# Kernel tuning notes

Measured on AMD Instinct MI355X. Metric: run time of the kernel, lower is better.

## Reference

```python
import jax, jax.numpy as jnp
import numpy as np

N_SPLIT = 4096   # split tokens (coarse octree levels)
N_VQ    = 12288  # VQ tokens (finest level)
N       = N_SPLIT + N_VQ
C       = 256    # num_embed
H       = 8      # num_heads
L       = 4      # num_blocks
P       = 256    # patch_size (attention window)
DIL     = 2      # dilation for odd (swin) blocks
DVQ     = 32     # vqvae embedding_channels
VQ_SIZE = 256    # vqvae embedding_sizes
VQ_G    = 4      # vqvae quantizer_group
HID     = 4 * C


def _layernorm(x, s, b):
    m = x.mean(-1, keepdims=True)
    v = jnp.var(x, axis=-1, keepdims=True)
    return (x - m) * jax.lax.rsqrt(v + 1e-5) * s + b


def _sin_pos_emb(n, c):
    pos = jnp.arange(n, dtype=jnp.float32)[:, None]
    half = c // 2
    freqs = jnp.exp(-jnp.log(10000.0) * jnp.arange(half, dtype=jnp.float32) / half)
    ang = pos * freqs
    return jnp.concatenate([jnp.sin(ang), jnp.cos(ang)], axis=-1)


def _forward(split, zq, targets_vq, category, batch_id, mask, d2b,
             split_emb, class_emb, vq_proj_w, vq_proj_b,
             ln1_s, ln1_b, qkv_w, qkv_b, attn_w, attn_b,
             ln2_s, ln2_b, fc1_w, fc1_b, fc2_w, fc2_b,
             lnx_s, lnx_b, split_w, split_b, vq_w, vq_b):
    # token embeddings: [split tokens ; projected VQ codes]
    x = jnp.concatenate([split_emb[split], zq @ vq_proj_w + vq_proj_b], axis=0)  # [N,C]
    cond = class_emb[category]                      # [B,C]
    x = jnp.where(mask[:, None], cond[batch_id], x)  # masked tokens -> class cond

    # depth2batch gather, then OctFormer blocks
    xb = x[d2b] + _sin_pos_emb(N, C).astype(x.dtype)
    dh = C // H
    scale = dh ** -0.5
    for l in range(L):
        d = DIL if (l % 2 == 1) else 1  # swin-style alternating dilation
        h = _layernorm(xb, ln1_s[l], ln1_b[l])
        # dilated window partition: window j in a super-window holds tokens base+p*d+j
        hw = h.reshape(-1, P, d, C).transpose(0, 2, 1, 3).reshape(-1, P, C)
        qkv = hw @ qkv_w[l] + qkv_b[l]              # [nw,P,3C]
        q, k, v = [t.reshape(-1, P, H, dh) for t in jnp.split(qkv, 3, axis=-1)]
        att = jax.nn.softmax(jnp.einsum('wphd,wqhd->whpq', q, k) * scale, axis=-1)
        o = jnp.einsum('whpq,wqhd->wphd', att, v).reshape(-1, P, C) @ attn_w[l] + attn_b[l]
        o = o.reshape(-1, d, P, C).transpose(0, 2, 1, 3).reshape(-1, C)  # undo partition
        xb = xb + o
        h = _layernorm(xb, ln2_s[l], ln2_b[l])
        xb = xb + (jax.nn.gelu(h @ fc1_w[l] + fc1_b[l]) @ fc2_w[l] + fc2_b[l])
    # batch2depth scatter (inverse permutation)
    x = jnp.zeros_like(xb).at[d2b].set(xb)
    x = _layernorm(x, lnx_s, lnx_b)

    # split head + masked cross-entropy
    sl = x[:N_SPLIT] @ split_w + split_b            # [Ns,2]
    ms = mask[:N_SPLIT].astype(jnp.float32)
    ce_s = -jnp.take_along_axis(jax.nn.log_softmax(sl, axis=-1), split[:, None], axis=-1)[:, 0]
    split_loss = jnp.sum(ce_s * ms) / jnp.maximum(jnp.sum(ms), 1.0)

    # vq head + masked grouped cross-entropy
    vl = (x[N_SPLIT:] @ vq_w + vq_b).reshape(N_VQ, VQ_G, VQ_SIZE)
    mv = mask[N_SPLIT:].astype(jnp.float32)
    ce_v = -jnp.take_along_axis(jax.nn.log_softmax(vl, axis=-1), targets_vq[..., None], axis=-1)[..., 0]
    vq_loss = jnp.sum(ce_v.mean(-1) * mv) / jnp.maximum(jnp.sum(mv), 1.0)
    return jnp.stack([split_loss, vq_loss])


def setup_inputs() -> dict:
    key = jax.random.key(0)
    ks = jax.random.split(key, 16)
    s = 0.02
    inp = {
        'split': jax.random.randint(ks[0], (N_SPLIT,), 0, 2),
        'zq': jax.random.normal(ks[1], (N_VQ, DVQ), jnp.float32),
        'targets_vq': jax.random.randint(ks[2], (N_VQ, VQ_G), 0, VQ_SIZE),
        'category': jnp.zeros((1,), jnp.int32),
        'batch_id': jnp.zeros((N,), jnp.int32),
        'mask': jax.random.randint(ks[3], (N,), 0, 2).astype(bool),
        'd2b': jax.random.permutation(ks[4], N),
        'split_emb': s * jax.random.normal(ks[5], (2, C), jnp.float32),
        'class_emb': s * jax.random.normal(ks[6], (1, C), jnp.float32),
        'vq_proj_w': s * jax.random.normal(ks[7], (DVQ, C), jnp.float32),
        'vq_proj_b': jnp.zeros((C,), jnp.float32),
        'ln1_s': jnp.ones((L, C), jnp.float32),
        'ln1_b': jnp.zeros((L, C), jnp.float32),
        'qkv_w': s * jax.random.normal(ks[8], (L, C, 3 * C), jnp.float32),
        'qkv_b': jnp.zeros((L, 3 * C), jnp.float32),
        'attn_w': s * jax.random.normal(ks[9], (L, C, C), jnp.float32),
        'attn_b': jnp.zeros((L, C), jnp.float32),
        'ln2_s': jnp.ones((L, C), jnp.float32),
        'ln2_b': jnp.zeros((L, C), jnp.float32),
        'fc1_w': s * jax.random.normal(ks[10], (L, C, HID), jnp.float32),
        'fc1_b': jnp.zeros((L, HID), jnp.float32),
        'fc2_w': s * jax.random.normal(ks[11], (L, HID, C), jnp.float32),
        'fc2_b': jnp.zeros((L, C), jnp.float32),
        'lnx_s': jnp.ones((C,), jnp.float32),
        'lnx_b': jnp.zeros((C,), jnp.float32),
        'split_w': s * jax.random.normal(ks[12], (C, 2), jnp.float32),
        'split_b': jnp.zeros((2,), jnp.float32),
        'vq_w': s * jax.random.normal(ks[13], (C, VQ_G * VQ_SIZE), jnp.float32),
        'vq_b': jnp.zeros((VQ_G * VQ_SIZE,), jnp.float32),
    }
    return inp


def reference(split, zq, targets_vq, category, batch_id, mask, d2b,
              split_emb, class_emb, vq_proj_w, vq_proj_b,
              ln1_s, ln1_b, qkv_w, qkv_b, attn_w, attn_b,
              ln2_s, ln2_b, fc1_w, fc1_b, fc2_w, fc2_b,
              lnx_s, lnx_b, split_w, split_b, vq_w, vq_b):
    return _forward(split, zq, targets_vq, category, batch_id, mask, d2b,
                    split_emb, class_emb, vq_proj_w, vq_proj_b,
                    ln1_s, ln1_b, qkv_w, qkv_b, attn_w, attn_b,
                    ln2_s, ln2_b, fc1_w, fc1_b, fc2_w, fc2_b,
                    lnx_s, lnx_b, split_w, split_b, vq_w, vq_b)
```

## Files before the change

### kernel.cpp

```cpp
#include <hip/hip_runtime.h>
#include <hip/hip_bf16.h>
#include <math.h>

#define NSPLIT 4096
#define NVQ    12288
#define NTOK   16384
#define CH     256
#define NH     8
#define DHD    32
#define NL     4
#define PW     256
#define HIDN   1024
#define DVQ    32
#define VQG    4
#define VQS    256

typedef __attribute__((ext_vector_type(8))) short bf16x8;
typedef __attribute__((ext_vector_type(4))) float f32x4;

typedef const __attribute__((address_space(1))) void* gas_ptr;
typedef __attribute__((address_space(3))) void* las_ptr;
#define GLD16(g, s) __builtin_amdgcn_global_load_lds((gas_ptr)(g), (las_ptr)(s), 16, 0, 0)

static __device__ __forceinline__ unsigned pack2bf(float a, float b) {
    __hip_bfloat16 ha = __float2bfloat16(a), hb = __float2bfloat16(b);
    return ((unsigned)*(unsigned short*)&hb << 16) | *(unsigned short*)&ha;
}
static __device__ __forceinline__ float bf2f(unsigned short s) {
    unsigned u = (unsigned)s << 16;
    return *(float*)&u;
}
static __device__ __forceinline__ unsigned short f2bfu(float f) {
    __hip_bfloat16 h = __float2bfloat16(f);
    return *(unsigned short*)&h;
}

__global__ void k_wt_all(const float* __restrict__ qkv_w, const float* __restrict__ attn_w,
                         const float* __restrict__ fc1_w, const float* __restrict__ fc2_w,
                         const float* __restrict__ vq_w,
                         short* __restrict__ qkvT, short* __restrict__ attnT,
                         short* __restrict__ fc1T, short* __restrict__ fc2T,
                         short* __restrict__ vqT,
                         const void* __restrict__ mask_raw, int* __restrict__ mode) {
    int b = blockIdx.x;
    if (b == 832) {
        __shared__ int c_even, c_odd, c_0100;
        const unsigned short* u16 = (const unsigned short*)mask_raw;
        if (threadIdx.x == 0) { c_even = 0; c_odd = 0; c_0100 = 0; }
        __syncthreads();
        int le = 0, lo = 0, l01 = 0;
        for (int i = threadIdx.x; i < 8192; i += 256) {
            unsigned short v = u16[i];
            if (v == 0x3F80u) { if (i & 1) lo++; else le++; }
            if (v == 0x0100u) l01++;
        }
        atomicAdd(&c_even, le); atomicAdd(&c_odd, lo); atomicAdd(&c_0100, l01);
        __syncthreads();
        if (threadIdx.x == 0) {
            int m;
            if      (c_even > 500) m = 2;
            else if (c_odd  > 500) m = 3;
            else if (c_0100 > 500) m = 1;
            else                   m = 0;
            *mode = m;
        }
        return;
    }
    const float* W; short* Wt; int K, N, tn, tk;
    if (b < 192)      { int r = b;       int z = r / 48; r %= 48; K = 256;  N = 768;
                        tk = r / 12; tn = r % 12;
                        W = qkv_w + (size_t)z * K * N; Wt = qkvT + (size_t)z * K * N; }
    else if (b < 256) { int r = b - 192; int z = r / 16; r %= 16; K = 256;  N = 256;
                        tk = r / 4;  tn = r % 4;
                        W = attn_w + (size_t)z * K * N; Wt = attnT + (size_t)z * K * N; }
    else if (b < 512) { int r = b - 256; int z = r / 64; r %= 64; K = 256;  N = 1024;
                        tk = r / 16; tn = r % 16;
                        W = fc1_w + (size_t)z * K * N; Wt = fc1T + (size_t)z * K * N; }
    else if (b < 768) { int r = b - 512; int z = r / 64; r %= 64; K = 1024; N = 256;
                        tk = r / 4;  tn = r % 4;
                        W = fc2_w + (size_t)z * K * N; Wt = fc2T + (size_t)z * K * N; }
    else              { int r = b - 768; K = 256; N = 1024;
                        tk = r / 16; tn = r % 16; W = vq_w; Wt = vqT; }
    __shared__ float t[64][65];
    int bn = tn * 64, bk = tk * 64, tid = threadIdx.x;
#pragma unroll
    for (int it = 0; it < 16; ++it) {
        int idx = it * 256 + tid; int r = idx >> 6, c = idx & 63;
        t[r][c] = W[(size_t)(bk + r) * N + bn + c];
    }
    __syncthreads();
#pragma unroll
    for (int it = 0; it < 16; ++it) {
        int idx = it * 256 + tid; int r = idx >> 6, c = idx & 63;
        __hip_bfloat16 h = __float2bfloat16(t[c][r]);
        Wt[(size_t)(bn + r) * K + bk + c] = *(short*)&h;
    }
}

__global__ void k_embed_gather(const int* __restrict__ split, const float* __restrict__ zq,
                               const int* __restrict__ category, const int* __restrict__ batch_id,
                               const void* __restrict__ mask_raw, const int* __restrict__ mode,
                               int* __restrict__ mask_i, const int* __restrict__ d2b,
                               const float* __restrict__ split_emb, const float* __restrict__ class_emb,
                               const float* __restrict__ vq_proj_w, const float* __restrict__ vq_proj_b,
                               const float* __restrict__ ln1s, const float* __restrict__ ln1b,
                               unsigned short* __restrict__ xbv, unsigned short* __restrict__ hb) {
    int j = blockIdx.x, c = threadIdx.x;
    int i = d2b[j];
    int m = *mode, mv;
    if      (m == 0) mv = ((const int*)mask_raw)[i] != 0;
    else if (m == 1) mv = ((const unsigned char*)mask_raw)[i] != 0;
    else if (m == 2) mv = ((const unsigned short*)mask_raw)[i] != 0;
    else             mv = ((const unsigned int*)mask_raw)[i] != 0;
    if (c == 0) mask_i[i] = mv;
    float v;
    if (mv) {
        v = class_emb[category[batch_id[i]] * CH + c];
    } else if (i < NSPLIT) {
        v = split_emb[split[i] * CH + c];
    } else {
        const float* z = zq + (size_t)(i - NSPLIT) * DVQ;
        float acc = vq_proj_b[c];
#pragma unroll
        for (int k = 0; k < DVQ; k++) acc += z[k] * vq_proj_w[k * CH + c];
        v = acc;
    }
    const float kneg = -0.07195578415606394f;
    float jf = (float)j, pe;
    if (c < 128) { float f = expf(c * kneg);         pe = sinf(jf * f); }
    else         { float f = expf((c - 128) * kneg); pe = cosf(jf * f); }
    v += pe;
    float s = v, sq = v * v;
#pragma unroll
    for (int o = 32; o; o >>= 1) { s += __shfl_xor(s, o); sq += __shfl_xor(sq, o); }
    __shared__ float ps[4], pq[4];
    if ((c & 63) == 0) { ps[c >> 6] = s; pq[c >> 6] = sq; }
    __syncthreads();
    float S = ps[0] + ps[1] + ps[2] + ps[3];
    float Q = pq[0] + pq[1] + pq[2] + pq[3];
    float mean = S * (1.0f / CH);
    float var  = Q * (1.0f / CH) - mean * mean;
    float rsf = rsqrtf(var + 1e-5f);
    xbv[(size_t)j * CH + c] = f2bfu(v);
    hb[(size_t)j * CH + c]  = f2bfu((v - mean) * rsf * ln1s[c] + ln1b[c]);
}

template <int GELU>
__global__ __launch_bounds__(256, 4) void k_mm(
    const short* __restrict__ A, const short* __restrict__ Bt,
    const float* __restrict__ bias, unsigned short* __restrict__ outB,
    int N, int K) {
    __shared__ short As[2][128 * 32];
    __shared__ short Bs[2][128 * 32];
    const int tid = threadIdx.x;
    const int w = tid >> 6, l = tid & 63;
    const int bm = blockIdx.y * 128, bn = blockIdx.x * 128;
    const int wr = w >> 1, wc = w & 1;
    const int q = l >> 4, rA = l & 15;
    const int srow = w * 16 + (l >> 2);
    const int sx = ((l & 3) ^ ((l >> 2) & 3)) * 8;
    const int fx = (q ^ (rA & 3)) * 8;

    const short* gA0 = A + (size_t)(bm + srow) * K + sx;
    const short* gA1 = A + (size_t)(bm + srow + 64) * K + sx;
    const short* gB0 = Bt + (size_t)(bn + srow) * K + sx;
    const short* gB1 = Bt + (size_t)(bn + srow + 64) * K + sx;
    short* lA0 = &As[0][w * 16 * 32];
    short* lA1 = &As[0][(64 + w * 16) * 32];
    short* lA0h = &As[1][w * 16 * 32];
    short* lA1h = &As[1][(64 + w * 16) * 32];
    short* lB0 = &Bs[0][w * 16 * 32];
    short* lB1 = &Bs[0][(64 + w * 16) * 32];
    short* lB0h = &Bs[1][w * 16 * 32];
    short* lB1h = &Bs[1][(64 + w * 16) * 32];

    f32x4 acc[4][4] = {};

    for (int k0 = 0; k0 < K; k0 += 64) {
        GLD16(gA0 + k0, lA0);       GLD16(gA1 + k0, lA1);
        GLD16(gA0 + k0 + 32, lA0h); GLD16(gA1 + k0 + 32, lA1h);
        GLD16(gB0 + k0, lB0);       GLD16(gB1 + k0, lB1);
        GLD16(gB0 + k0 + 32, lB0h); GLD16(gB1 + k0 + 32, lB1h);
        __syncthreads();
#pragma unroll
        for (int s = 0; s < 2; s++) {
            bf16x8 a[4], b[4];
#pragma unroll
            for (int m = 0; m < 4; m++)
                a[m] = *(const bf16x8*)(&As[s][(wr * 64 + m * 16 + rA) * 32 + fx]);
#pragma unroll
            for (int n = 0; n < 4; n++)
                b[n] = *(const bf16x8*)(&Bs[s][(wc * 64 + n * 16 + rA) * 32 + fx]);
#pragma unroll
            for (int m = 0; m < 4; m++)
#pragma unroll
                for (int n = 0; n < 4; n++)
                    acc[m][n] = __builtin_amdgcn_mfma_f32_16x16x32_bf16(b[n], a[m], acc[m][n], 0, 0, 0);
        }
        __syncthreads();
    }

#pragma unroll
    for (int m = 0; m < 4; m++) {
        int row = bm + wr * 64 + m * 16 + rA;
#pragma unroll
        for (int n = 0; n < 4; n++) {
            int colb = bn + wc * 64 + n * 16 + q * 4;
            float4 bv = *(const float4*)(bias + colb);
            float v0 = acc[m][n][0] + bv.x;
            float v1 = acc[m][n][1] + bv.y;
            float v2 = acc[m][n][2] + bv.z;
            float v3 = acc[m][n][3] + bv.w;
            if (GELU) {
                float t0 = tanhf(0.7978845608028654f * (v0 + 0.044715f * v0 * v0 * v0));
                float t1 = tanhf(0.7978845608028654f * (v1 + 0.044715f * v1 * v1 * v1));
                float t2 = tanhf(0.7978845608028654f * (v2 + 0.044715f * v2 * v2 * v2));
                float t3 = tanhf(0.7978845608028654f * (v3 + 0.044715f * v3 * v3 * v3));
                v0 = 0.5f * v0 * (1.0f + t0); v1 = 0.5f * v1 * (1.0f + t1);
                v2 = 0.5f * v2 * (1.0f + t2); v3 = 0.5f * v3 * (1.0f + t3);
            }
            ushort4 st = { f2bfu(v0), f2bfu(v1), f2bfu(v2), f2bfu(v3) };
            *(ushort4*)(outB + (size_t)row * N + colb) = st;
        }
    }
}

template <int LNOUT>
__global__ __launch_bounds__(256, 4) void k_mm_row(
    const short* __restrict__ A, const short* __restrict__ Bt,
    const float* __restrict__ bias, unsigned short* __restrict__ xbv,
    const float* __restrict__ lns, const float* __restrict__ lnb,
    unsigned short* __restrict__ h_out, const int* __restrict__ d2b, int K) {
    __shared__ short As[2][32 * 32];
    __shared__ short Bs[2][256 * 32];
    __shared__ float part[2][4][32];
    const int tid = threadIdx.x;
    const int w = tid >> 6, l = tid & 63;
    const int bm = blockIdx.x * 32;
    const int q = l >> 4, rA = l & 15;
    const int sx = ((l & 3) ^ ((l >> 2) & 3)) * 8;
    const int fx = (q ^ (rA & 3)) * 8;

    const short* gA = A + (size_t)(bm + (l >> 2)) * K + sx;
    const short* gB = Bt + (size_t)(w * 64 + (l >> 2)) * K + sx;

    f32x4 acc[2][4] = {};

    for (int k0 = 0; k0 < K; k0 += 64) {
        if (w == 0) {
#pragma unroll
            for (int rg = 0; rg < 2; rg++) {
                GLD16(gA + (size_t)(rg * 16) * K + k0,      &As[0][(rg * 16) * 32]);
                GLD16(gA + (size_t)(rg * 16) * K + k0 + 32, &As[1][(rg * 16) * 32]);
            }
        }
#pragma unroll
        for (int i = 0; i < 4; i++) {
            GLD16(gB + (size_t)(i * 16) * K + k0,      &Bs[0][(w * 64 + i * 16) * 32]);
            GLD16(gB + (size_t)(i * 16) * K + k0 + 32, &Bs[1][(w * 64 + i * 16) * 32]);
        }
        __syncthreads();
#pragma unroll
        for (int s = 0; s < 2; s++) {
            bf16x8 a[2], b[4];
#pragma unroll
            for (int m = 0; m < 2; m++)
                a[m] = *(const bf16x8*)(&As[s][(m * 16 + rA) * 32 + fx]);
#pragma unroll
            for (int n = 0; n < 4; n++)
                b[n] = *(const bf16x8*)(&Bs[s][(w * 64 + n * 16 + rA) * 32 + fx]);
#pragma unroll
            for (int m = 0; m < 2; m++)
#pragma unroll
                for (int n = 0; n < 4; n++)
                    acc[m][n] = __builtin_amdgcn_mfma_f32_16x16x32_bf16(b[n], a[m], acc[m][n], 0, 0, 0);
        }
        __syncthreads();
    }

    float rsum[2] = {}, rsq[2] = {};
#pragma unroll
    for (int m = 0; m < 2; m++) {
        int row = bm + m * 16 + rA;
#pragma unroll
        for (int n = 0; n < 4; n++) {
            int colb = w * 64 + n * 16 + q * 4;
            float4 bv = *(const float4*)(bias + colb);
            size_t oi = (size_t)row * CH + colb;
            ushort4 xo = *(const ushort4*)(xbv + oi);
            float v0 = acc[m][n][0] + bv.x + bf2f(xo.x);
            float v1 = acc[m][n][1] + bv.y + bf2f(xo.y);
            float v2 = acc[m][n][2] + bv.z + bf2f(xo.z);
            float v3 = acc[m][n][3] + bv.w + bf2f(xo.w);
            acc[m][n][0] = v0; acc[m][n][1] = v1; acc[m][n][2] = v2; acc[m][n][3] = v3;
            if (LNOUT != 2) {
                ushort4 st = { f2bfu(v0), f2bfu(v1), f2bfu(v2), f2bfu(v3) };
                *(ushort4*)(xbv + oi) = st;
            }
            rsum[m] += (v0 + v1) + (v2 + v3);
            rsq[m]  += (v0 * v0 + v1 * v1) + (v2 * v2 + v3 * v3);
        }
    }
    if (LNOUT) {
#pragma unroll
        for (int m = 0; m < 2; m++) {
            rsum[m] += __shfl_xor(rsum[m], 16); rsum[m] += __shfl_xor(rsum[m], 32);
            rsq[m]  += __shfl_xor(rsq[m], 16);  rsq[m]  += __shfl_xor(rsq[m], 32);
        }
        if (q == 0) {
#pragma unroll
            for (int m = 0; m < 2; m++) {
                part[0][w][m * 16 + rA] = rsum[m];
                part[1][w][m * 16 + rA] = rsq[m];
            }
        }
        __syncthreads();
#pragma unroll
        for (int m = 0; m < 2; m++) {
            int row = m * 16 + rA;
            float S = part[0][0][row] + part[0][1][row] + part[0][2][row] + part[0][3][row];
            float Q = part[1][0][row] + part[1][1][row] + part[1][2][row] + part[1][3][row];
            float mean = S * (1.0f / CH);
            float var  = Q * (1.0f / CH) - mean * mean;
            float rsf = rsqrtf(var + 1e-5f);
            size_t orow = (LNOUT == 2) ? (size_t)d2b[bm + row] : (size_t)(bm + row);
#pragma unroll
            for (int n = 0; n < 4; n++) {
                int colb = w * 64 + n * 16 + q * 4;
                float4 sv = *(const float4*)(lns + colb);
                float4 bb = *(const float4*)(lnb + colb);
                ushort4 st = {
                    f2bfu((acc[m][n][0] - mean) * rsf * sv.x + bb.x),
                    f2bfu((acc[m][n][1] - mean) * rsf * sv.y + bb.y),
                    f2bfu((acc[m][n][2] - mean) * rsf * sv.z + bb.z),
                    f2bfu((acc[m][n][3] - mean) * rsf * sv.w + bb.w) };
                *(ushort4*)(h_out + orow * CH + colb) = st;
            }
        }
    }
}

__global__ __launch_bounds__(256, 4) void k_vq_head(
    const short* __restrict__ A, const short* __restrict__ vqT,
    const float* __restrict__ vq_b, const int* __restrict__ targets,
    float* __restrict__ vce4) {
    __shared__ short As[2][32 * 32];
    __shared__ short Bs[2][256 * 32];
    __shared__ float part[2][4][32];
    __shared__ float tgtv[32];
    const int tid = threadIdx.x;
    const int w = tid >> 6, l = tid & 63;
    const int bm = blockIdx.x * 32;
    const int g = blockIdx.y;
    const int q = l >> 4, rA = l & 15;
    const int sx = ((l & 3) ^ ((l >> 2) & 3)) * 8;
    const int fx = (q ^ (rA & 3)) * 8;

    const short* gA = A + (size_t)(bm + (l >> 2)) * CH + sx;
    const short* gB = vqT + (size_t)(g * VQS + w * 64 + (l >> 2)) * CH + sx;

    f32x4 acc[2][4] = {};

    for (int k0 = 0; k0 < CH; k0 += 64) {
        if (w == 0) {
#pragma unroll
            for (int rg = 0; rg < 2; rg++) {
                GLD16(gA + (size_t)(rg * 16) * CH + k0,      &As[0][(rg * 16) * 32]);
                GLD16(gA + (size_t)(rg * 16) * CH + k0 + 32, &As[1][(rg * 16) * 32]);
            }
        }
#pragma unroll
        for (int i = 0; i < 4; i++) {
            GLD16(gB + (size_t)(i * 16) * CH + k0,      &Bs[0][(w * 64 + i * 16) * 32]);
            GLD16(gB + (size_t)(i * 16) * CH + k0 + 32, &Bs[1][(w * 64 + i * 16) * 32]);
        }
        __syncthreads();
#pragma unroll
        for (int s = 0; s < 2; s++) {
            bf16x8 a[2], b[4];
#pragma unroll
            for (int m = 0; m < 2; m++)
                a[m] = *(const bf16x8*)(&As[s][(m * 16 + rA) * 32 + fx]);
#pragma unroll
            for (int n = 0; n < 4; n++)
                b[n] = *(const bf16x8*)(&Bs[s][(w * 64 + n * 16 + rA) * 32 + fx]);
#pragma unroll
            for (int m = 0; m < 2; m++)
#pragma unroll
                for (int n = 0; n < 4; n++)
                    acc[m][n] = __builtin_amdgcn_mfma_f32_16x16x32_bf16(b[n], a[m], acc[m][n], 0, 0, 0);
        }
        __syncthreads();
    }

    float pm[2];
#pragma unroll
    for (int m = 0; m < 2; m++) {
        pm[m] = -1e30f;
        int row = m * 16 + rA;
        int t = targets[(size_t)(bm + row) * VQG + g];
#pragma unroll
        for (int n = 0; n < 4; n++) {
            int colb = w * 64 + n * 16 + q * 4;
            float4 bv = *(const float4*)(vq_b + g * VQS + colb);
            float v0 = acc[m][n][0] + bv.x;
            float v1 = acc[m][n][1] + bv.y;
            float v2 = acc[m][n][2] + bv.z;
            float v3 = acc[m][n][3] + bv.w;
            acc[m][n][0] = v0; acc[m][n][1] = v1; acc[m][n][2] = v2; acc[m][n][3] = v3;
            if (colb + 0 == t) tgtv[row] = v0;
            if (colb + 1 == t) tgtv[row] = v1;
            if (colb + 2 == t) tgtv[row] = v2;
            if (colb + 3 == t) tgtv[row] = v3;
            pm[m] = fmaxf(pm[m], fmaxf(fmaxf(v0, v1), fmaxf(v2, v3)));
        }
    }
#pragma unroll
    for (int m = 0; m < 2; m++) {
        pm[m] = fmaxf(pm[m], __shfl_xor(pm[m], 16));
        pm[m] = fmaxf(pm[m], __shfl_xor(pm[m], 32));
    }
    if (q == 0) {
#pragma unroll
        for (int m = 0; m < 2; m++) part[0][w][m * 16 + rA] = pm[m];
    }
    __syncthreads();
    float pmf[2], psum[2];
#pragma unroll
    for (int m = 0; m < 2; m++) {
        int row = m * 16 + rA;
        float mx = fmaxf(fmaxf(part[0][0][row], part[0][1][row]),
                         fmaxf(part[0][2][row], part[0][3][row]));
        pmf[m] = mx;
        float s = 0.f;
#pragma unroll
        for (int n = 0; n < 4; n++)
            s += __expf(acc[m][n][0] - mx) + __expf(acc[m][n][1] - mx)
               + __expf(acc[m][n][2] - mx) + __expf(acc[m][n][3] - mx);
        psum[m] = s;
    }
#pragma unroll
    for (int m = 0; m < 2; m++) {
        psum[m] += __shfl_xor(psum[m], 16);
        psum[m] += __shfl_xor(psum[m], 32);
    }
    if (q == 0) {
#pragma unroll
        for (int m = 0; m < 2; m++) part[1][w][m * 16 + rA] = psum[m];
    }
    __syncthreads();
    if (w == 0 && q == 0) {
#pragma unroll
        for (int m = 0; m < 2; m++) {
            int row = m * 16 + rA;
            float tot = part[1][0][row] + part[1][1][row] + part[1][2][row] + part[1][3][row];
            float lse = pmf[m] + logf(tot);
            vce4[(size_t)(bm + row) * VQG + g] = lse - tgtv[row];
        }
    }
}

__global__ __launch_bounds__(256) void k_attn_mfma(const short* __restrict__ qkv,
                                                   short* __restrict__ o, int dil) {
    __shared__ short Vt[DHD * PW];
    __shared__ short Kl[PW * DHD];
    __shared__ short Pl[4][64 * 64];
    const int wid = blockIdx.x, h = blockIdx.y;
    const int tid = threadIdx.x;
    const int w = tid >> 6, l = tid & 63;
    const int g = l >> 4, c = l & 15;
    const int tbase = (wid / dil) * (PW * dil) + (wid % dil);

#pragma unroll
    for (int j2 = 0; j2 < 4; j2++) {
        int row = j2 * 64 + w * 16 + (l >> 2);
        int sc = (l & 3) ^ (row & 3);
        GLD16(qkv + (size_t)(tbase + row * dil) * 768 + CH + h * DHD + sc * 8,
              Kl + (j2 * 64 + w * 16) * DHD);
    }

    {
        const int p = tid;
        const short* src = qkv + (size_t)(tbase + p * dil) * 768 + 2 * CH + h * DHD;
        bf16x8 v0 = *(const bf16x8*)(src);
        bf16x8 v1 = *(const bf16x8*)(src + 8);
        bf16x8 v2 = *(const bf16x8*)(src + 16);
        bf16x8 v3 = *(const bf16x8*)(src + 24);
        const int pc = p >> 3, po = p & 7;
#pragma unroll
        for (int d = 0; d < 8; d++)  Vt[(d)      * PW + ((pc ^ d) << 3) + po] = v0[d];
#pragma unroll
        for (int d = 0; d < 8; d++)  Vt[(d + 8)  * PW + ((pc ^ d) << 3) + po] = v1[d];
#pragma unroll
        for (int d = 0; d < 8; d++)  Vt[(d + 16) * PW + ((pc ^ d) << 3) + po] = v2[d];
#pragma unroll
        for (int d = 0; d < 8; d++)  Vt[(d + 24) * PW + ((pc ^ d) << 3) + po] = v3[d];
    }

    bf16x8 qf[4];
#pragma unroll
    for (int qt = 0; qt < 4; qt++) {
        int qrow = w * 64 + qt * 16 + c;
        qf[qt] = *(const bf16x8*)(qkv + (size_t)(tbase + qrow * dil) * 768 + h * DHD + g * 8);
    }

    f32x4 acco[4][2] = {};
    float m_s[4] = {-1e30f, -1e30f, -1e30f, -1e30f};
    float l_s[4] = {0.f, 0.f, 0.f, 0.f};
    const float scale = 0.17677669529663687f;

    __syncthreads();

#pragma unroll
    for (int ch = 0; ch < 4; ch++) {
        bf16x8 kf[4];
#pragma unroll
        for (int kvt = 0; kvt < 4; kvt++) {
            int kv = ch * 64 + kvt * 16 + c;
            kf[kvt] = *(const bf16x8*)(Kl + kv * DHD + ((g ^ (c & 3)) * 8));
        }
        f32x4 accs[4][4] = {};
#pragma unroll
        for (int kvt = 0; kvt < 4; kvt++)
#pragma unroll
            for (int qt = 0; qt < 4; qt++)
                accs[kvt][qt] = __builtin_amdgcn_mfma_f32_16x16x32_bf16(kf[kvt], qf[qt], accs[kvt][qt], 0, 0, 0);

        float fb[4];
#pragma unroll
        for (int qt = 0; qt < 4; qt++) {
            float mx = -1e30f;
#pragma unroll
            for (int kvt = 0; kvt < 4; kvt++) {
                mx = fmaxf(mx, fmaxf(fmaxf(accs[kvt][qt][0], accs[kvt][qt][1]),
                                     fmaxf(accs[kvt][qt][2], accs[kvt][qt][3])));
            }
            mx = fmaxf(mx, __shfl_xor(mx, 16));
            mx = fmaxf(mx, __shfl_xor(mx, 32));
            float mnew = fmaxf(m_s[qt], mx * scale);
            fb[qt] = __expf(m_s[qt] - mnew);
            m_s[qt] = mnew;
        }
#pragma unroll
        for (int mt = 0; mt < 4; mt++) {
            float fo = fb[mt];
#pragma unroll
            for (int r = 0; r < 4; r++) {
                acco[mt][0][r] *= fo;
                acco[mt][1][r] *= fo;
            }
        }
        float rsum[4] = {0.f, 0.f, 0.f, 0.f};
#pragma unroll
        for (int kvt = 0; kvt < 4; kvt++) {
            const int cchunk = kvt * 2 + (g >> 1);
            const int koff = (g & 1) << 2;
#pragma unroll
            for (int qt = 0; qt < 4; qt++) {
                float p0 = __expf(accs[kvt][qt][0] * scale - m_s[qt]);
                float p1 = __expf(accs[kvt][qt][1] * scale - m_s[qt]);
                float p2 = __expf(accs[kvt][qt][2] * scale - m_s[qt]);
                float p3 = __expf(accs[kvt][qt][3] * scale - m_s[qt]);
                rsum[qt] += (p0 + p1) + (p2 + p3);
                int qq = qt * 16 + c;
                int phys = cchunk ^ (qq & 7);
                uint2 pk; pk.x = pack2bf(p0, p1); pk.y = pack2bf(p2, p3);
                *(uint2*)(&Pl[w][qq * 64 + phys * 8 + koff]) = pk;
            }
        }
#pragma unroll
        for (int qt = 0; qt < 4; qt++) {
            float s = rsum[qt];
            s += __shfl_xor(s, 16);
            s += __shfl_xor(s, 32);
            l_s[qt] = l_s[qt] * fb[qt] + s;
        }
#pragma unroll
        for (int ks = 0; ks < 2; ks++) {
            bf16x8 pa[4];
#pragma unroll
            for (int mt = 0; mt < 4; mt++) {
                int qq = mt * 16 + c;
                int phys = (ks * 4 + g) ^ (qq & 7);
                pa[mt] = *(const bf16x8*)(&Pl[w][qq * 64 + phys * 8]);
            }
#pragma unroll
            for (int nt = 0; nt < 2; nt++) {
                int d = nt * 16 + c;
                int kvabs = ch * 64 + ks * 32 + g * 8;
                int phys = (kvabs >> 3) ^ (d & 7);
                bf16x8 vb = *(const bf16x8*)(&Vt[d * PW + phys * 8]);
#pragma unroll
                for (int mt = 0; mt < 4; mt++)
                    acco[mt][nt] = __builtin_amdgcn_mfma_f32_16x16x32_bf16(vb, pa[mt], acco[mt][nt], 0, 0, 0);
            }
        }
    }

#pragma unroll
    for (int mt = 0; mt < 4; mt++) {
        float linv = 1.0f / l_s[mt];
        int qrow = w * 64 + mt * 16 + c;
        size_t trow = (size_t)(tbase + qrow * dil) * CH + h * DHD;
#pragma unroll
        for (int nt = 0; nt < 2; nt++) {
            ushort4 st = { f2bfu(acco[mt][nt][0] * linv), f2bfu(acco[mt][nt][1] * linv),
                           f2bfu(acco[mt][nt][2] * linv), f2bfu(acco[mt][nt][3] * linv) };
            *(ushort4*)((unsigned short*)o + trow + nt * 16 + g * 4) = st;
        }
    }
}

__global__ void k_split_mini(const unsigned short* __restrict__ h, const int* __restrict__ split,
                             const int* __restrict__ mask_i, const float* __restrict__ sw,
                             const float* __restrict__ sb, float* __restrict__ sce) {
    int i = blockIdx.x * 4 + (threadIdx.x >> 6);
    int l = threadIdx.x & 63;
    ushort4 uv = *(const ushort4*)(h + (size_t)i * CH + l * 4);
    float n0 = bf2f(uv.x), n1 = bf2f(uv.y), n2 = bf2f(uv.z), n3 = bf2f(uv.w);
    int c0 = l * 4;
    float a0 = n0 * sw[2 * c0] + n1 * sw[2 * (c0 + 1)] + n2 * sw[2 * (c0 + 2)] + n3 * sw[2 * (c0 + 3)];
    float a1 = n0 * sw[2 * c0 + 1] + n1 * sw[2 * (c0 + 1) + 1] + n2 * sw[2 * (c0 + 2) + 1] + n3 * sw[2 * (c0 + 3) + 1];
#pragma unroll
    for (int o = 32; o; o >>= 1) { a0 += __shfl_xor(a0, o); a1 += __shfl_xor(a1, o); }
    if (l == 0) {
        float l0 = a0 + sb[0], l1 = a1 + sb[1];
        float mx = fmaxf(l0, l1);
        float lse = mx + logf(__expf(l0 - mx) + __expf(l1 - mx));
        float ce = lse - (split[i] ? l1 : l0);
        sce[i] = ce * (float)mask_i[i];
    }
}

__global__ void k_reduce(const float* __restrict__ sce, const float* __restrict__ vce4,
                         const int* __restrict__ mask_i, float* __restrict__ out) {
    int tid = threadIdx.x;
    float s1 = 0, s2 = 0, s3 = 0, s4 = 0;
    for (int i = tid; i < NSPLIT; i += 256) { s1 += sce[i]; s2 += (float)mask_i[i]; }
    for (int i = tid; i < NVQ; i += 256) {
        float mv = (float)mask_i[NSPLIT + i];
        float cs = vce4[i * 4 + 0] + vce4[i * 4 + 1] + vce4[i * 4 + 2] + vce4[i * 4 + 3];
        s3 += cs * 0.25f * mv;
        s4 += mv;
    }
    __shared__ float r1[256], r2[256], r3[256], r4[256];
    r1[tid] = s1; r2[tid] = s2; r3[tid] = s3; r4[tid] = s4;
    __syncthreads();
    for (int o = 128; o; o >>= 1) {
        if (tid < o) { r1[tid] += r1[tid + o]; r2[tid] += r2[tid + o];
                       r3[tid] += r3[tid + o]; r4[tid] += r4[tid + o]; }
        __syncthreads();
    }
    if (tid == 0) {
        out[0] = r1[0] / fmaxf(r2[0], 1.0f);
        out[1] = r3[0] / fmaxf(r4[0], 1.0f);
    }
}

extern "C" void kernel_launch(void* const* d_in, const int* in_sizes, int n_in,
                              void* d_out, int out_size, void* d_ws, size_t ws_size,
                              hipStream_t stream) {
    const int*   split      = (const int*)d_in[0];
    const float* zq         = (const float*)d_in[1];
    const int*   targets_vq = (const int*)d_in[2];
    const int*   category   = (const int*)d_in[3];
    const int*   batch_id   = (const int*)d_in[4];
    const void*  mask_raw   = d_in[5];
    const int*   d2b        = (const int*)d_in[6];
    const float* split_emb  = (const float*)d_in[7];
    const float* class_emb  = (const float*)d_in[8];
    const float* vq_proj_w  = (const float*)d_in[9];
    const float* vq_proj_b  = (const float*)d_in[10];
    const float* ln1_s      = (const float*)d_in[11];
    const float* ln1_b      = (const float*)d_in[12];
    const float* qkv_w      = (const float*)d_in[13];
    const float* qkv_b      = (const float*)d_in[14];
    const float* attn_w     = (const float*)d_in[15];
    const float* attn_b     = (const float*)d_in[16];
    const float* ln2_s      = (const float*)d_in[17];
    const float* ln2_b      = (const float*)d_in[18];
    const float* fc1_w      = (const float*)d_in[19];
    const float* fc1_b      = (const float*)d_in[20];
    const float* fc2_w      = (const float*)d_in[21];
    const float* fc2_b      = (const float*)d_in[22];
    const float* lnx_s      = (const float*)d_in[23];
    const float* lnx_b      = (const float*)d_in[24];
    const float* sw         = (const float*)d_in[25];
    const float* sb         = (const float*)d_in[26];
    const float* vq_w       = (const float*)d_in[27];
    const float* vq_b       = (const float*)d_in[28];

    char* ws = (char*)d_ws;
    int* mode   = (int*)ws;
    int* mask_i = (int*)(ws + 256);
    float* sce  = (float*)(ws + 256 + 4 * NTOK);
    float* vce4 = sce + NSPLIT;
    char* p = ws + (1 << 20);
    short* qkvT = (short*)p;  p += (size_t)NL * 768 * CH * 2;
    short* attnT = (short*)p; p += (size_t)NL * CH * CH * 2;
    short* fc1T = (short*)p;  p += (size_t)NL * HIDN * CH * 2;
    short* fc2T = (short*)p;  p += (size_t)NL * CH * HIDN * 2;
    short* vqT = (short*)p;   p += (size_t)HIDN * CH * 2;
    unsigned short* xbv = (unsigned short*)p; p += (size_t)NTOK * CH * 2;
    unsigned short* h_bf = (unsigned short*)p; p += (size_t)NTOK * CH * 2;
    unsigned short* o_bf = (unsigned short*)p; p += (size_t)NTOK * CH * 2;
    short* big = (short*)p;

    k_wt_all<<<833, 256, 0, stream>>>(qkv_w, attn_w, fc1_w, fc2_w, vq_w,
                                      qkvT, attnT, fc1T, fc2T, vqT, mask_raw, mode);
    k_embed_gather<<<NTOK, 256, 0, stream>>>(split, zq, category, batch_id, mask_raw, mode,
                                             mask_i, d2b, split_emb, class_emb,
                                             vq_proj_w, vq_proj_b, ln1_s, ln1_b, xbv, h_bf);

    for (int l = 0; l < NL; l++) {
        int d = (l & 1) ? 2 : 1;
        k_mm<0><<<dim3(768 / 128, NTOK / 128), 256, 0, stream>>>(
            (const short*)h_bf, qkvT + (size_t)l * 768 * CH, qkv_b + l * 768,
            (unsigned short*)big, 768, CH);
        k_attn_mfma<<<dim3(NTOK / PW, NH), 256, 0, stream>>>(big, (short*)o_bf, d);
        k_mm_row<1><<<NTOK / 32, 256, 0, stream>>>(
            (const short*)o_bf, attnT + (size_t)l * CH * CH, attn_b + l * CH,
            xbv, ln2_s + l * CH, ln2_b + l * CH, h_bf, nullptr, CH);
        k_mm<1><<<dim3(HIDN / 128, NTOK / 128), 256, 0, stream>>>(
            (const short*)h_bf, fc1T + (size_t)l * HIDN * CH, fc1_b + l * HIDN,
            (unsigned short*)big, HIDN, CH);
        if (l < NL - 1) {
            k_mm_row<1><<<NTOK / 32, 256, 0, stream>>>(
                big, fc2T + (size_t)l * CH * HIDN, fc2_b + l * CH,
                xbv, ln1_s + (l + 1) * CH, ln1_b + (l + 1) * CH, h_bf, nullptr, HIDN);
        } else {
            k_mm_row<2><<<NTOK / 32, 256, 0, stream>>>(
                big, fc2T + (size_t)l * CH * HIDN, fc2_b + l * CH,
                xbv, lnx_s, lnx_b, h_bf, d2b, HIDN);
        }
    }

    k_split_mini<<<NSPLIT / 4, 256, 0, stream>>>(h_bf, split, mask_i, sw, sb, sce);
    k_vq_head<<<dim3(NVQ / 32, VQG), 256, 0, stream>>>(
        (const short*)(h_bf + (size_t)NSPLIT * CH), vqT, vq_b, targets_vq, vce4);
    k_reduce<<<1, 256, 0, stream>>>(sce, vce4, mask_i, (float*)d_out);
}
```

Before: 481.8 us.

## Fuse split-head loss into final LN epilogue and use 8-wave attention blocks

The final fc2+LayerNorm kernel now computes the split-token logits and cross-entropy directly from the fp32 normalized values, so the separate k_split_mini launch and its re-read of h are removed. The attention kernel moves from 4 to 8 waves per block, each wave handling 32 query rows instead of 64. This halves per-wave register state and splits the K/V loads across more threads, aiming for better latency hiding. The LDS buffer for P is reshaped to match. The fused loss uses unrounded fp32 activations rather than bf16, which slightly changes numerics.

```diff
diff --git a/kernel.cpp b/kernel.cpp
--- a/kernel.cpp
+++ b/kernel.cpp
@@ -230,7 +230,10 @@
     const short* __restrict__ A, const short* __restrict__ Bt,
     const float* __restrict__ bias, unsigned short* __restrict__ xbv,
     const float* __restrict__ lns, const float* __restrict__ lnb,
-    unsigned short* __restrict__ h_out, const int* __restrict__ d2b, int K) {
+    unsigned short* __restrict__ h_out, const int* __restrict__ d2b, int K,
+    const int* __restrict__ split, const int* __restrict__ mask_i,
+    const float* __restrict__ sw, const float* __restrict__ sb,
+    float* __restrict__ sce) {
     __shared__ short As[2][32 * 32];
     __shared__ short Bs[2][256 * 32];
     __shared__ float part[2][4][32];
@@ -329,12 +332,54 @@
                 int colb = w * 64 + n * 16 + q * 4;
                 float4 sv = *(const float4*)(lns + colb);
                 float4 bb = *(const float4*)(lnb + colb);
-                ushort4 st = {
-                    f2bfu((acc[m][n][0] - mean) * rsf * sv.x + bb.x),
-                    f2bfu((acc[m][n][1] - mean) * rsf * sv.y + bb.y),
-                    f2bfu((acc[m][n][2] - mean) * rsf * sv.z + bb.z),
-                    f2bfu((acc[m][n][3] - mean) * rsf * sv.w + bb.w) };
+                float h0 = (acc[m][n][0] - mean) * rsf * sv.x + bb.x;
+                float h1 = (acc[m][n][1] - mean) * rsf * sv.y + bb.y;
+                float h2 = (acc[m][n][2] - mean) * rsf * sv.z + bb.z;
+                float h3 = (acc[m][n][3] - mean) * rsf * sv.w + bb.w;
+                acc[m][n][0] = h0; acc[m][n][1] = h1; acc[m][n][2] = h2; acc[m][n][3] = h3;
+                ushort4 st = { f2bfu(h0), f2bfu(h1), f2bfu(h2), f2bfu(h3) };
                 *(ushort4*)(h_out + orow * CH + colb) = st;
+            }
+        }
+    }
+    if (LNOUT == 2) {
+        float a0[2] = {}, a1[2] = {};
+#pragma unroll
+        for (int m = 0; m < 2; m++) {
+#pragma unroll
+            for (int n = 0; n < 4; n++) {
+                int colb = w * 64 + n * 16 + q * 4;
+#pragma unroll
+                for (int j = 0; j < 4; j++) {
+                    a0[m] += acc[m][n][j] * sw[2 * (colb + j)];
+                    a1[m] += acc[m][n][j] * sw[2 * (colb + j) + 1];
+                }
+            }
+            a0[m] += __shfl_xor(a0[m], 16); a0[m] += __shfl_xor(a0[m], 32);
+            a1[m] += __shfl_xor(a1[m], 16); a1[m] += __shfl_xor(a1[m], 32);
+        }
+        __syncthreads();
+        if (q == 0) {
+#pragma unroll
+            for (int m = 0; m < 2; m++) {
+                part[0][w][m * 16 + rA] = a0[m];
+                part[1][w][m * 16 + rA] = a1[m];
+            }
+        }
+        __syncthreads();
+        if (w == 0 && q == 0) {
+#pragma unroll
+            for (int m = 0; m < 2; m++) {
+                int row = m * 16 + rA;
+                int orow = d2b[bm + row];
+                if (orow < NSPLIT) {
+                    float l0 = part[0][0][row] + part[0][1][row] + part[0][2][row] + part[0][3][row] + sb[0];
+                    float l1 = part[1][0][row] + part[1][1][row] + part[1][2][row] + part[1][3][row] + sb[1];
+                    float mx = fmaxf(l0, l1);
+                    float lse = mx + logf(__expf(l0 - mx) + __expf(l1 - mx));
+                    float ce = lse - (split[orow] ? l1 : l0);
+                    sce[orow] = ce * (float)mask_i[orow];
+                }
             }
         }
     }
@@ -460,11 +505,11 @@
     }
 }
 
-__global__ __launch_bounds__(256) void k_attn_mfma(const short* __restrict__ qkv,
-                                                   short* __restrict__ o, int dil) {
+__global__ __launch_bounds__(512, 4) void k_attn_mfma(const short* __restrict__ qkv,
+                                                      short* __restrict__ o, int dil) {
     __shared__ short Vt[DHD * PW];
     __shared__ short Kl[PW * DHD];
-    __shared__ short Pl[4][64 * 64];
+    __shared__ short Pl[8][32 * 64];
     const int wid = blockIdx.x, h = blockIdx.y;
     const int tid = threadIdx.x;
     const int w = tid >> 6, l = tid & 63;
@@ -472,41 +517,37 @@
     const int tbase = (wid / dil) * (PW * dil) + (wid % dil);
 
 #pragma unroll
-    for (int j2 = 0; j2 < 4; j2++) {
-        int row = j2 * 64 + w * 16 + (l >> 2);
+    for (int j2 = 0; j2 < 2; j2++) {
+        int row = j2 * 128 + w * 16 + (l >> 2);
         int sc = (l & 3) ^ (row & 3);
         GLD16(qkv + (size_t)(tbase + row * dil) * 768 + CH + h * DHD + sc * 8,
-              Kl + (j2 * 64 + w * 16) * DHD);
+              Kl + (j2 * 128 + w * 16) * DHD);
     }
 
     {
-        const int p = tid;
-        const short* src = qkv + (size_t)(tbase + p * dil) * 768 + 2 * CH + h * DHD;
+        const int p = tid >> 1, half = tid & 1;
+        const short* src = qkv + (size_t)(tbase + p * dil) * 768 + 2 * CH + h * DHD + half * 16;
         bf16x8 v0 = *(const bf16x8*)(src);
         bf16x8 v1 = *(const bf16x8*)(src + 8);
-        bf16x8 v2 = *(const bf16x8*)(src + 16);
-        bf16x8 v3 = *(const bf16x8*)(src + 24);
         const int pc = p >> 3, po = p & 7;
 #pragma unroll
-        for (int d = 0; d < 8; d++)  Vt[(d)      * PW + ((pc ^ d) << 3) + po] = v0[d];
-#pragma unroll
-        for (int d = 0; d < 8; d++)  Vt[(d + 8)  * PW + ((pc ^ d) << 3) + po] = v1[d];
-#pragma unroll
-        for (int d = 0; d < 8; d++)  Vt[(d + 16) * PW + ((pc ^ d) << 3) + po] = v2[d];
-#pragma unroll
-        for (int d = 0; d < 8; d++)  Vt[(d + 24) * PW + ((pc ^ d) << 3) + po] = v3[d];
-    }
-
-    bf16x8 qf[4];
-#pragma unroll
-    for (int qt = 0; qt < 4; qt++) {
-        int qrow = w * 64 + qt * 16 + c;
+        for (int d = 0; d < 8; d++)
+            Vt[(half * 16 + d) * PW + ((pc ^ d) << 3) + po] = v0[d];
+#pragma unroll
+        for (int d = 0; d < 8; d++)
+            Vt[(half * 16 + 8 + d) * PW + ((pc ^ d) << 3) + po] = v1[d];
+    }
+
+    bf16x8 qf[2];
+#pragma unroll
+    for (int qt = 0; qt < 2; qt++) {
+        int qrow = w * 32 + qt * 16 + c;
         qf[qt] = *(const bf16x8*)(qkv + (size_t)(tbase + qrow * dil) * 768 + h * DHD + g * 8);
     }
 
-    f32x4 acco[4][2] = {};
-    float m_s[4] = {-1e30f, -1e30f, -1e30f, -1e30f};
-    float l_s[4] = {0.f, 0.f, 0.f, 0.f};
+    f32x4 acco[2][2] = {};
+    float m_s[2] = {-1e30f, -1e30f};
+    float l_s[2] = {0.f, 0.f};
     const float scale = 0.17677669529663687f;
 
     __syncthreads();
@@ -519,16 +560,16 @@
             int kv = ch * 64 + kvt * 16 + c;
             kf[kvt] = *(const bf16x8*)(Kl + kv * DHD + ((g ^ (c & 3)) * 8));
         }
-        f32x4 accs[4][4] = {};
+        f32x4 accs[4][2] = {};
 #pragma unroll
         for (int kvt = 0; kvt < 4; kvt++)
 #pragma unroll
-            for (int qt = 0; qt < 4; qt++)
+            for (int qt = 0; qt < 2; qt++)
                 accs[kvt][qt] = __builtin_amdgcn_mfma_f32_16x16x32_bf16(kf[kvt], qf[qt], accs[kvt][qt], 0, 0, 0);
 
-        float fb[4];
-#pragma unroll
-        for (int qt = 0; qt < 4; qt++) {
+        float fb[2];
+#pragma unroll
+        for (int qt = 0; qt < 2; qt++) {
             float mx = -1e30f;
 #pragma unroll
             for (int kvt = 0; kvt < 4; kvt++) {
@@ -542,7 +583,7 @@
             m_s[qt] = mnew;
         }
 #pragma unroll
-        for (int mt = 0; mt < 4; mt++) {
+        for (int mt = 0; mt < 2; mt++) {
             float fo = fb[mt];
 #pragma unroll
             for (int r = 0; r < 4; r++) {
@@ -550,13 +591,13 @@
                 acco[mt][1][r] *= fo;
             }
         }
-        float rsum[4] = {0.f, 0.f, 0.f, 0.f};
+        float rsum[2] = {0.f, 0.f};
 #pragma unroll
         for (int kvt = 0; kvt < 4; kvt++) {
             const int cchunk = kvt * 2 + (g >> 1);
             const int koff = (g & 1) << 2;
 #pragma unroll
-            for (int qt = 0; qt < 4; qt++) {
+            for (int qt = 0; qt < 2; qt++) {
                 float p0 = __expf(accs[kvt][qt][0] * scale - m_s[qt]);
                 float p1 = __expf(accs[kvt][qt][1] * scale - m_s[qt]);
                 float p2 = __expf(accs[kvt][qt][2] * scale - m_s[qt]);
@@ -569,7 +610,7 @@
             }
         }
 #pragma unroll
-        for (int qt = 0; qt < 4; qt++) {
+        for (int qt = 0; qt < 2; qt++) {
             float s = rsum[qt];
             s += __shfl_xor(s, 16);
             s += __shfl_xor(s, 32);
@@ -577,9 +618,9 @@
         }
 #pragma unroll
         for (int ks = 0; ks < 2; ks++) {
-            bf16x8 pa[4];
-#pragma unroll
-            for (int mt = 0; mt < 4; mt++) {
+            bf16x8 pa[2];
+#pragma unroll
+            for (int mt = 0; mt < 2; mt++) {
                 int qq = mt * 16 + c;
                 int phys = (ks * 4 + g) ^ (qq & 7);
                 pa[mt] = *(const bf16x8*)(&Pl[w][qq * 64 + phys * 8]);
@@ -591,16 +632,16 @@
                 int phys = (kvabs >> 3) ^ (d & 7);
                 bf16x8 vb = *(const bf16x8*)(&Vt[d * PW + phys * 8]);
 #pragma unroll
-                for (int mt = 0; mt < 4; mt++)
+                for (int mt = 0; mt < 2; mt++)
                     acco[mt][nt] = __builtin_amdgcn_mfma_f32_16x16x32_bf16(vb, pa[mt], acco[mt][nt], 0, 0, 0);
             }
         }
     }
 
 #pragma unroll
-    for (int mt = 0; mt < 4; mt++) {
+    for (int mt = 0; mt < 2; mt++) {
         float linv = 1.0f / l_s[mt];
-        int qrow = w * 64 + mt * 16 + c;
+        int qrow = w * 32 + mt * 16 + c;
         size_t trow = (size_t)(tbase + qrow * dil) * CH + h * DHD;
 #pragma unroll
         for (int nt = 0; nt < 2; nt++) {
@@ -608,27 +649,6 @@
                            f2bfu(acco[mt][nt][2] * linv), f2bfu(acco[mt][nt][3] * linv) };
             *(ushort4*)((unsigned short*)o + trow + nt * 16 + g * 4) = st;
         }
-    }
-}
-
-__global__ void k_split_mini(const unsigned short* __restrict__ h, const int* __restrict__ split,
-                             const int* __restrict__ mask_i, const float* __restrict__ sw,
-                             const float* __restrict__ sb, float* __restrict__ sce) {
-    int i = blockIdx.x * 4 + (threadIdx.x >> 6);
-    int l = threadIdx.x & 63;
-    ushort4 uv = *(const ushort4*)(h + (size_t)i * CH + l * 4);
-    float n0 = bf2f(uv.x), n1 = bf2f(uv.y), n2 = bf2f(uv.z), n3 = bf2f(uv.w);
-    int c0 = l * 4;
-    float a0 = n0 * sw[2 * c0] + n1 * sw[2 * (c0 + 1)] + n2 * sw[2 * (c0 + 2)] + n3 * sw[2 * (c0 + 3)];
-    float a1 = n0 * sw[2 * c0 + 1] + n1 * sw[2 * (c0 + 1) + 1] + n2 * sw[2 * (c0 + 2) + 1] + n3 * sw[2 * (c0 + 3) + 1];
-#pragma unroll
-    for (int o = 32; o; o >>= 1) { a0 += __shfl_xor(a0, o); a1 += __shfl_xor(a1, o); }
-    if (l == 0) {
-        float l0 = a0 + sb[0], l1 = a1 + sb[1];
-        float mx = fmaxf(l0, l1);
-        float lse = mx + logf(__expf(l0 - mx) + __expf(l1 - mx));
-        float ce = lse - (split[i] ? l1 : l0);
-        sce[i] = ce * (float)mask_i[i];
     }
 }
 
@@ -717,25 +737,27 @@
         k_mm<0><<<dim3(768 / 128, NTOK / 128), 256, 0, stream>>>(
             (const short*)h_bf, qkvT + (size_t)l * 768 * CH, qkv_b + l * 768,
             (unsigned short*)big, 768, CH);
-        k_attn_mfma<<<dim3(NTOK / PW, NH), 256, 0, stream>>>(big, (short*)o_bf, d);
+        k_attn_mfma<<<dim3(NTOK / PW, NH), 512, 0, stream>>>(big, (short*)o_bf, d);
         k_mm_row<1><<<NTOK / 32, 256, 0, stream>>>(
             (const short*)o_bf, attnT + (size_t)l * CH * CH, attn_b + l * CH,
-            xbv, ln2_s + l * CH, ln2_b + l * CH, h_bf, nullptr, CH);
+            xbv, ln2_s + l * CH, ln2_b + l * CH, h_bf, nullptr, CH,
+            nullptr, nullptr, nullptr, nullptr, nullptr);
         k_mm<1><<<dim3(HIDN / 128, NTOK / 128), 256, 0, stream>>>(
             (const short*)h_bf, fc1T + (size_t)l * HIDN * CH, fc1_b + l * HIDN,
             (unsigned short*)big, HIDN, CH);
         if (l < NL - 1) {
             k_mm_row<1><<<NTOK / 32, 256, 0, stream>>>(
                 big, fc2T + (size_t)l * CH * HIDN, fc2_b + l * CH,
-                xbv, ln1_s + (l + 1) * CH, ln1_b + (l + 1) * CH, h_bf, nullptr, HIDN);
+                xbv, ln1_s + (l + 1) * CH, ln1_b + (l + 1) * CH, h_bf, nullptr, HIDN,
+                nullptr, nullptr, nullptr, nullptr, nullptr);
         } else {
             k_mm_row<2><<<NTOK / 32, 256, 0, stream>>>(
                 big, fc2T + (size_t)l * CH * HIDN, fc2_b + l * CH,
-                xbv, lnx_s, lnx_b, h_bf, d2b, HIDN);
-        }
-    }
-
-    k_split_mini<<<NSPLIT / 4, 256, 0, stream>>>(h_bf, split, mask_i, sw, sb, sce);
+                xbv, lnx_s, lnx_b, h_bf, d2b, HIDN,
+                split, mask_i, sw, sb, sce);
+        }
+    }
+
     k_vq_head<<<dim3(NVQ / 32, VQG), 256, 0, stream>>>(
         (const short*)(h_bf + (size_t)NSPLIT * CH), vqT, vq_b, targets_vq, vce4);
     k_reduce<<<1, 256, 0, stream>>>(sce, vce4, mask_i, (float*)d_out);
```

Measured after the change: 467.0 us. -3.1%, faster.
